# Performance work log

Measured on AMD Instinct MI355X. Metric: run time of the kernel, lower is better.

The kernel has to match this reference:

```python
import jax, jax.numpy as jnp
import numpy as np

EPS = 1e-7
LAMBDA_COORD = 10.0
LAMBDA_NOOBJ = 0.5
LAMBDA_OBJ = 1.0


def setup_inputs() -> dict:
    key = jax.random.key(0)
    k1, k2, k3, k4 = jax.random.split(key, 4)
    B, A, C, G = 64, 3, 20, 76
    predictions = jax.random.normal(k1, (B, A * (5 + C), G, G), dtype=jnp.float32) * 0.5
    txy = jax.random.uniform(k2, (B, A, G, G, 2), dtype=jnp.float32)
    twh = jax.random.normal(k3, (B, A, G, G, 2), dtype=jnp.float32) * 0.3
    tconf = (jax.random.uniform(k4, (B, A, G, G, 1), dtype=jnp.float32) < 0.05).astype(jnp.float32)
    targets = jnp.concatenate([txy, twh, tconf], axis=-1)
    anchors = jnp.array([[1.25, 1.625], [2.0, 3.75], [4.125, 2.875]], dtype=jnp.float32)
    return {"predictions": predictions, "targets": targets, "anchors": anchors}


def _bce(p, t):
    # elementwise binary cross-entropy; p in (0,1) from sigmoid
    return -(t * jnp.log(p) + (1.0 - t) * jnp.log1p(-p))


def _ciou_loss_elem(pb, tb):
    # pb, tb: [..., 4] corner boxes; returns elementwise (1 - ciou)
    x1p, y1p, x2p, y2p = pb[..., 0], pb[..., 1], pb[..., 2], pb[..., 3]
    x1t, y1t, x2t, y2t = tb[..., 0], tb[..., 1], tb[..., 2], tb[..., 3]
    iw = jnp.clip(jnp.minimum(x2p, x2t) - jnp.maximum(x1p, x1t), 0.0)
    ih = jnp.clip(jnp.minimum(y2p, y2t) - jnp.maximum(y1p, y1t), 0.0)
    inter = iw * ih
    area_p = jnp.clip(x2p - x1p, 0.0) * jnp.clip(y2p - y1p, 0.0)
    area_t = jnp.clip(x2t - x1t, 0.0) * jnp.clip(y2t - y1t, 0.0)
    union = area_p + area_t - inter + EPS
    iou = inter / union
    rho2 = ((x1p + x2p - x1t - x2t) * 0.5) ** 2 + ((y1p + y2p - y1t - y2t) * 0.5) ** 2
    en_w = jnp.clip(jnp.maximum(x2p, x2t) - jnp.minimum(x1p, x1t), EPS)
    en_h = jnp.clip(jnp.maximum(y2p, y2t) - jnp.minimum(y1p, y1t), EPS)
    c2 = en_w ** 2 + en_h ** 2
    w_p = jnp.clip(x2p - x1p, EPS); h_p = jnp.clip(y2p - y1p, EPS)
    w_t = jnp.clip(x2t - x1t, EPS); h_t = jnp.clip(y2t - y1t, EPS)
    v = (4.0 / (jnp.pi ** 2)) * (jnp.arctan(w_t / h_t) - jnp.arctan(w_p / h_p)) ** 2
    alpha = jax.lax.stop_gradient(v / (1.0 - iou + v + EPS))
    ciou = iou - rho2 / (c2 + EPS) - alpha * v
    return 1.0 - ciou


def reference(predictions, targets, anchors):
    B, Ch, G, _ = predictions.shape
    A = anchors.shape[0]
    C = Ch // A - 5
    p = predictions.reshape(B, A, 5 + C, G, G).transpose(0, 1, 3, 4, 2)  # [B,A,G,G,5+C]
    pred_xy = jax.nn.sigmoid(p[..., :2])
    pred_wh = p[..., 2:4]
    pred_conf = jax.nn.sigmoid(p[..., 4])
    pred_cls = jax.nn.sigmoid(p[..., 5:])
    obj = targets[..., 4] > 0          # [B,A,G,G]
    n_obj = jnp.sum(obj.astype(jnp.float32))
    n_noobj = jnp.sum((~obj).astype(jnp.float32))
    gy, gx = jnp.meshgrid(jnp.arange(G, dtype=jnp.float32), jnp.arange(G, dtype=jnp.float32), indexing='ij')
    inv_g = 1.0 / G
    aw = anchors[:, 0][None, :, None, None] * inv_g
    ah = anchors[:, 1][None, :, None, None] * inv_g
    # predicted corner boxes
    pcx = (gx + pred_xy[..., 0]) * inv_g
    pcy = (gy + pred_xy[..., 1]) * inv_g
    pw = jnp.exp(pred_wh[..., 0]) * aw
    ph = jnp.exp(pred_wh[..., 1]) * ah
    pred_corners = jnp.clip(jnp.stack([pcx - pw / 2, pcy - ph / 2, pcx + pw / 2, pcy + ph / 2], axis=-1), 0.0, 1.0)
    # target corner boxes
    tcx = (gx + targets[..., 0]) * inv_g
    tcy = (gy + targets[..., 1]) * inv_g
    tw = jnp.exp(targets[..., 2]) * aw
    th = jnp.exp(targets[..., 3]) * ah
    tgt_corners = jnp.clip(jnp.stack([tcx - tw / 2, tcy - th / 2, tcx + tw / 2, tcy + th / 2], axis=-1), 0.0, 1.0)
    ciou_l = _ciou_loss_elem(pred_corners, tgt_corners)  # [B,A,G,G]
    coord_sum = jnp.sum(jnp.where(obj, ciou_l, 0.0))
    coord_loss = jnp.where(n_obj > 0, coord_sum / jnp.maximum(n_obj, 1.0), 0.0)
    conf_bce = _bce(pred_conf, targets[..., 4])
    obj_loss = jnp.where(n_obj > 0, jnp.sum(jnp.where(obj, conf_bce, 0.0)) / jnp.maximum(n_obj, 1.0), 0.0)
    noobj_bce = -jnp.log1p(-pred_conf)  # BCE with target 0
    noobj_loss = jnp.where(n_noobj > 0, jnp.sum(jnp.where(~obj, noobj_bce, 0.0)) / jnp.maximum(n_noobj, 1.0), 0.0)
    if C > 0:
        cls_bce = -jnp.log(pred_cls)  # BCE with target 1
        cls_sum = jnp.sum(jnp.where(obj[..., None], cls_bce, 0.0))
        class_loss = jnp.where(n_obj > 0, cls_sum / jnp.maximum(n_obj * C, 1.0), 0.0)
    else:
        class_loss = jnp.float32(0.0)
    total = LAMBDA_COORD * coord_loss + LAMBDA_OBJ * obj_loss + LAMBDA_NOOBJ * noobj_loss + class_loss
    return total
```

## Files before the change

### kernel.cpp

```cpp
#include <hip/hip_runtime.h>
#include <math.h>

namespace {

constexpr int   kB     = 64;
constexpr int   kA     = 3;
constexpr int   kC     = 20;
constexpr int   kG     = 76;
constexpr int   kGG    = kG * kG;
constexpr int   kCH    = 5 + kC;
constexpr int   kNCell = kB * kA * kGG;
constexpr int   kNC4   = kNCell / 4;
constexpr int   kBlockA = 256;
constexpr int   kGridA  = kNC4 / kBlockA;
constexpr int   kCellsPerBlk = kBlockA * 4;
constexpr float kEps   = 1e-7f;
constexpr float kInvG  = 1.0f / (float)kG;

constexpr int kPart1Off = kGridA;
constexpr int kPart2Off = kGridA * 5;
constexpr int kListOff  = kGridA * 7;

__device__ __forceinline__ float softplus_fast(float x) {
  return fmaxf(x, 0.0f) + __logf(1.0f + __expf(-fabsf(x)));
}
__device__ __forceinline__ float sigmoidf(float x) {
  return 1.0f / (1.0f + __expf(-x));
}
__device__ __forceinline__ float clamp01(float x) {
  return fminf(fmaxf(x, 0.0f), 1.0f);
}

__device__ __forceinline__ void heavy_cell(
    int cell, const float* __restrict__ preds, const float* __restrict__ tgts,
    const float* __restrict__ anchors, float& coord, float& cls) {
  const int ba = cell / kGG;
  const int j  = cell - ba * kGG;
  const int a  = ba % kA;
  const int gy = j / kG;
  const int gx = j - gy * kG;
  const float fgx = (float)gx, fgy = (float)gy;

  const float aw = anchors[2 * a]     * kInvG;
  const float ah = anchors[2 * a + 1] * kInvG;

  const float* pb = preds + (size_t)ba * kCH * kGG + j;
  const float px  = pb[0];
  const float py  = pb[(size_t)1 * kGG];
  const float pwv = pb[(size_t)2 * kGG];
  const float phv = pb[(size_t)3 * kGG];

  const float* tc5 = tgts + (size_t)cell * 5;
  const float tx = tc5[0], ty = tc5[1], tw = tc5[2], th = tc5[3];

  const float pcx = (fgx + sigmoidf(px)) * kInvG;
  const float pcy = (fgy + sigmoidf(py)) * kInvG;
  const float pw  = __expf(pwv) * aw;
  const float ph  = __expf(phv) * ah;
  const float x1p = clamp01(pcx - 0.5f * pw);
  const float y1p = clamp01(pcy - 0.5f * ph);
  const float x2p = clamp01(pcx + 0.5f * pw);
  const float y2p = clamp01(pcy + 0.5f * ph);

  const float tcx = (fgx + tx) * kInvG;
  const float tcy = (fgy + ty) * kInvG;
  const float twv = __expf(tw) * aw;
  const float thv = __expf(th) * ah;
  const float x1t = clamp01(tcx - 0.5f * twv);
  const float y1t = clamp01(tcy - 0.5f * thv);
  const float x2t = clamp01(tcx + 0.5f * twv);
  const float y2t = clamp01(tcy + 0.5f * thv);

  const float iw     = fmaxf(fminf(x2p, x2t) - fmaxf(x1p, x1t), 0.0f);
  const float ih     = fmaxf(fminf(y2p, y2t) - fmaxf(y1p, y1t), 0.0f);
  const float inter  = iw * ih;
  const float area_p = fmaxf(x2p - x1p, 0.0f) * fmaxf(y2p - y1p, 0.0f);
  const float area_t = fmaxf(x2t - x1t, 0.0f) * fmaxf(y2t - y1t, 0.0f);
  const float uni    = area_p + area_t - inter + kEps;
  const float iou    = inter / uni;
  const float dx     = (x1p + x2p - x1t - x2t) * 0.5f;
  const float dy     = (y1p + y2p - y1t - y2t) * 0.5f;
  const float rho2   = dx * dx + dy * dy;
  const float enw    = fmaxf(fmaxf(x2p, x2t) - fminf(x1p, x1t), kEps);
  const float enh    = fmaxf(fmaxf(y2p, y2t) - fminf(y1p, y1t), kEps);
  const float c2     = enw * enw + enh * enh;
  const float wp     = fmaxf(x2p - x1p, kEps);
  const float hp     = fmaxf(y2p - y1p, kEps);
  const float wt     = fmaxf(x2t - x1t, kEps);
  const float ht     = fmaxf(y2t - y1t, kEps);
  const float k4pi2  = 4.0f / (float)(M_PI * M_PI);
  const float dat    = atanf(wt / ht) - atanf(wp / hp);
  const float v      = k4pi2 * dat * dat;
  const float alpha  = v / (1.0f - iou + v + kEps);
  const float ciou   = iou - rho2 / (c2 + kEps) - alpha * v;
  coord += 1.0f - ciou;

  float cacc = 0.0f;
  #pragma unroll
  for (int c = 0; c < kC; ++c) {
    cacc += softplus_fast(-pb[(size_t)(5 + c) * kGG]);
  }
  cls += cacc;
}

template <int N, int BLK>
__device__ __forceinline__ void block_reduceN(float r[N], float* out) {
  #pragma unroll
  for (int off = 32; off > 0; off >>= 1) {
    #pragma unroll
    for (int s = 0; s < N; ++s) r[s] += __shfl_down(r[s], off, 64);
  }
  __shared__ float red[BLK / 64][N];
  const int lane = threadIdx.x & 63;
  const int wid  = threadIdx.x >> 6;
  if (lane == 0) {
    #pragma unroll
    for (int s = 0; s < N; ++s) red[wid][s] = r[s];
  }
  __syncthreads();
  if (threadIdx.x == 0) {
    #pragma unroll
    for (int s = 0; s < N; ++s) {
      float acc = red[0][s];
      #pragma unroll
      for (int w = 1; w < BLK / 64; ++w) acc += red[w][s];
      out[s] = acc;
    }
  }
}

__global__ __launch_bounds__(kBlockA) void yolo_pass1(
    const float* __restrict__ preds,
    const float* __restrict__ tgts,
    const float* __restrict__ anchors,
    int* __restrict__ ws_i,
    int cap) {
  const int b    = blockIdx.x;
  const int q    = b * kBlockA + threadIdx.x;
  const int cell = q * 4;
  const int ba   = cell / kGG;
  const int j0   = cell - ba * kGG;

  const float4* tb = (const float4*)(tgts + (size_t)cell * 5);
  const float4 t1 = tb[1], t2 = tb[2], t3 = tb[3], t4 = tb[4];
  const float conf[4] = { t1.x, t2.y, t3.z, t4.w };

  const float* p4p = preds + (size_t)ba * kCH * kGG + (size_t)4 * kGG + j0;
  const float4 P4 = *(const float4*)p4p;
  const float p4a[4] = { P4.x, P4.y, P4.z, P4.w };

  float r[4] = {0.f, 0.f, 0.f, 0.f};
  unsigned msk = 0u;

  #pragma unroll
  for (int i = 0; i < 4; ++i) {
    const bool obj = conf[i] > 0.0f;
    const float sp = softplus_fast(p4a[i]);
    if (obj) {
      r[0] += sp - p4a[i];
      msk |= (1u << i);
    } else {
      r[1] += sp;
    }
  }
  const int cnt = __popc(msk);

  const int lane = threadIdx.x & 63;
  const int wid  = threadIdx.x >> 6;
  int incl = cnt;
  #pragma unroll
  for (int off = 1; off < 64; off <<= 1) {
    const int n = __shfl_up(incl, off, 64);
    if (lane >= off) incl += n;
  }
  const int excl = incl - cnt;

  __shared__ int wtot[kBlockA / 64];
  if (lane == 63) wtot[wid] = incl;
  __syncthreads();

  int wbase = 0;
  #pragma unroll
  for (int w = 0; w < kBlockA / 64; ++w) wbase += (w < wid) ? wtot[w] : 0;
  const int total = wtot[0] + wtot[1] + wtot[2] + wtot[3];

  if (threadIdx.x == 0) ws_i[b] = total;

  int* list = ws_i + kListOff + (size_t)b * cap;
  int p = wbase + excl;
  #pragma unroll
  for (int i = 0; i < 4; ++i) {
    if ((msk >> i) & 1u) {
      if (p < cap) {
        list[p] = cell + i;
      } else {
        heavy_cell(cell + i, preds, tgts, anchors, r[2], r[3]);
      }
      ++p;
    }
  }

  block_reduceN<4, kBlockA>(r, (float*)(ws_i + kPart1Off) + (size_t)b * 4);
}

__global__ __launch_bounds__(64) void yolo_pass2(
    const float* __restrict__ preds,
    const float* __restrict__ tgts,
    const float* __restrict__ anchors,
    int* __restrict__ ws_i,
    int cap) {
  const int b   = blockIdx.x;
  const int cnt = min(ws_i[b], cap);
  const int* list = ws_i + kListOff + (size_t)b * cap;

  float coord = 0.0f, cls = 0.0f;
  for (int i = threadIdx.x; i < cnt; i += 64) {
    heavy_cell(list[i], preds, tgts, anchors, coord, cls);
  }

  #pragma unroll
  for (int off = 32; off > 0; off >>= 1) {
    coord += __shfl_down(coord, off, 64);
    cls   += __shfl_down(cls,   off, 64);
  }
  if (threadIdx.x == 0) {
    float* p2 = (float*)(ws_i + kPart2Off) + (size_t)b * 2;
    p2[0] = coord;
    p2[1] = cls;
  }
}

__global__ __launch_bounds__(256) void yolo_finish(
    const int* __restrict__ ws_i, float* __restrict__ out) {
  const float* part1 = (const float*)(ws_i + kPart1Off);
  const float* part2 = (const float*)(ws_i + kPart2Off);

  float r[7] = {0.f, 0.f, 0.f, 0.f, 0.f, 0.f, 0.f};
  for (int i = threadIdx.x; i < kGridA; i += 256) {
    r[0] += (float)ws_i[i];
    r[1] += part1[(size_t)i * 4 + 0];
    r[2] += part1[(size_t)i * 4 + 1];
    r[3] += part1[(size_t)i * 4 + 2];
    r[4] += part1[(size_t)i * 4 + 3];
    r[5] += part2[(size_t)i * 2 + 0];
    r[6] += part2[(size_t)i * 2 + 1];
  }
  __shared__ float outbuf[7];
  block_reduceN<7, 256>(r, outbuf);
  __syncthreads();
  if (threadIdx.x == 0) {
    const float n_obj   = outbuf[0];
    const float objc    = outbuf[1];
    const float noobj   = outbuf[2];
    const float coord   = outbuf[3] + outbuf[5];
    const float cls     = outbuf[4] + outbuf[6];
    const float n_noobj = (float)kNCell - n_obj;

    const float coord_loss = (n_obj > 0.f)   ? coord / fmaxf(n_obj, 1.f)   : 0.f;
    const float obj_loss   = (n_obj > 0.f)   ? objc  / fmaxf(n_obj, 1.f)   : 0.f;
    const float noobj_loss = (n_noobj > 0.f) ? noobj / fmaxf(n_noobj, 1.f) : 0.f;
    const float class_loss = (n_obj > 0.f)   ? cls / fmaxf(n_obj * (float)kC, 1.f) : 0.f;

    out[0] = 10.0f * coord_loss + 1.0f * obj_loss + 0.5f * noobj_loss + class_loss;
  }
}

}

extern "C" void kernel_launch(void* const* d_in, const int* in_sizes, int n_in,
                              void* d_out, int out_size, void* d_ws, size_t ws_size,
                              hipStream_t stream) {
  const float* preds   = (const float*)d_in[0];
  const float* tgts    = (const float*)d_in[1];
  const float* anchors = (const float*)d_in[2];
  float* out = (float*)d_out;
  int*   ws  = (int*)d_ws;

  long words = (long)(ws_size / 4) - kListOff;
  int cap = (int)(words / kGridA);
  if (cap > kCellsPerBlk) cap = kCellsPerBlk;
  if (cap < 0) cap = 0;

  yolo_pass1<<<kGridA, kBlockA, 0, stream>>>(preds, tgts, anchors, ws, cap);
  yolo_pass2<<<kGridA, 64, 0, stream>>>(preds, tgts, anchors, ws, cap);
  yolo_finish<<<1, 256, 0, stream>>>(ws, out);
}
```

Before: 31.90 us.

## Fuse compaction and heavy CIoU pass into one kernel with LDS work list

Merges the two pass kernels into one. Each block compacts its object cells and their target xywh into shared memory, then processes that list with all 256 threads instead of a separate 64-thread kernel reading a global list. This drops a kernel launch, the global list round trip and the re-read of targets. It also replaces atanf and the precise divisions with a polynomial arctangent and fast divides, which changes numerical accuracy slightly.

```diff
diff --git a/kernel.cpp b/kernel.cpp
--- a/kernel.cpp
+++ b/kernel.cpp
@@ -16,10 +16,9 @@
 constexpr int   kCellsPerBlk = kBlockA * 4;
 constexpr float kEps   = 1e-7f;
 constexpr float kInvG  = 1.0f / (float)kG;
-
-constexpr int kPart1Off = kGridA;
-constexpr int kPart2Off = kGridA * 5;
-constexpr int kListOff  = kGridA * 7;
+constexpr float kPiO2  = 1.57079632679f;
+
+constexpr int kPartOff = kGridA;
 
 __device__ __forceinline__ float softplus_fast(float x) {
   return fmaxf(x, 0.0f) + __logf(1.0f + __expf(-fabsf(x)));
@@ -31,9 +30,22 @@
   return fminf(fmaxf(x, 0.0f), 1.0f);
 }
 
+__device__ __forceinline__ float atan_ratio(float num, float den) {
+  const float z  = __fdividef(fminf(num, den), fmaxf(num, den));
+  const float z2 = z * z;
+  float p = 0.0208351f;
+  p = fmaf(p, z2, -0.0851330f);
+  p = fmaf(p, z2,  0.1801410f);
+  p = fmaf(p, z2, -0.3302995f);
+  p = fmaf(p, z2,  0.9998660f);
+  const float a = z * p;
+  return (num > den) ? (kPiO2 - a) : a;
+}
+
 __device__ __forceinline__ void heavy_cell(
-    int cell, const float* __restrict__ preds, const float* __restrict__ tgts,
-    const float* __restrict__ anchors, float& coord, float& cls) {
+    int cell, float tx, float ty, float tw, float th,
+    const float* __restrict__ preds, const float* __restrict__ anchors,
+    float& coord, float& cls) {
   const int ba = cell / kGG;
   const int j  = cell - ba * kGG;
   const int a  = ba % kA;
@@ -49,9 +61,6 @@
   const float py  = pb[(size_t)1 * kGG];
   const float pwv = pb[(size_t)2 * kGG];
   const float phv = pb[(size_t)3 * kGG];
-
-  const float* tc5 = tgts + (size_t)cell * 5;
-  const float tx = tc5[0], ty = tc5[1], tw = tc5[2], th = tc5[3];
 
   const float pcx = (fgx + sigmoidf(px)) * kInvG;
   const float pcy = (fgy + sigmoidf(py)) * kInvG;
@@ -77,7 +86,7 @@
   const float area_p = fmaxf(x2p - x1p, 0.0f) * fmaxf(y2p - y1p, 0.0f);
   const float area_t = fmaxf(x2t - x1t, 0.0f) * fmaxf(y2t - y1t, 0.0f);
   const float uni    = area_p + area_t - inter + kEps;
-  const float iou    = inter / uni;
+  const float iou    = __fdividef(inter, uni);
   const float dx     = (x1p + x2p - x1t - x2t) * 0.5f;
   const float dy     = (y1p + y2p - y1t - y2t) * 0.5f;
   const float rho2   = dx * dx + dy * dy;
@@ -89,10 +98,10 @@
   const float wt     = fmaxf(x2t - x1t, kEps);
   const float ht     = fmaxf(y2t - y1t, kEps);
   const float k4pi2  = 4.0f / (float)(M_PI * M_PI);
-  const float dat    = atanf(wt / ht) - atanf(wp / hp);
+  const float dat    = atan_ratio(wt, ht) - atan_ratio(wp, hp);
   const float v      = k4pi2 * dat * dat;
-  const float alpha  = v / (1.0f - iou + v + kEps);
-  const float ciou   = iou - rho2 / (c2 + kEps) - alpha * v;
+  const float alpha  = __fdividef(v, 1.0f - iou + v + kEps);
+  const float ciou   = iou - __fdividef(rho2, c2 + kEps) - alpha * v;
   coord += 1.0f - ciou;
 
   float cacc = 0.0f;
@@ -129,21 +138,25 @@
   }
 }
 
-__global__ __launch_bounds__(kBlockA) void yolo_pass1(
+__global__ __launch_bounds__(kBlockA) void yolo_fused(
     const float* __restrict__ preds,
     const float* __restrict__ tgts,
     const float* __restrict__ anchors,
-    int* __restrict__ ws_i,
-    int cap) {
+    int* __restrict__ ws_i) {
+  __shared__ int    s_list[kCellsPerBlk];
+  __shared__ float4 s_tgt[kCellsPerBlk];
+  __shared__ int    s_wtot[kBlockA / 64];
+
   const int b    = blockIdx.x;
   const int q    = b * kBlockA + threadIdx.x;
   const int cell = q * 4;
   const int ba   = cell / kGG;
   const int j0   = cell - ba * kGG;
 
+  union { float4 v[5]; float f[20]; } T;
   const float4* tb = (const float4*)(tgts + (size_t)cell * 5);
-  const float4 t1 = tb[1], t2 = tb[2], t3 = tb[3], t4 = tb[4];
-  const float conf[4] = { t1.x, t2.y, t3.z, t4.w };
+  #pragma unroll
+  for (int i = 0; i < 5; ++i) T.v[i] = tb[i];
 
   const float* p4p = preds + (size_t)ba * kCH * kGG + (size_t)4 * kGG + j0;
   const float4 P4 = *(const float4*)p4p;
@@ -154,7 +167,7 @@
 
   #pragma unroll
   for (int i = 0; i < 4; ++i) {
-    const bool obj = conf[i] > 0.0f;
+    const bool obj = T.f[i * 5 + 4] > 0.0f;
     const float sp = softplus_fast(p4a[i]);
     if (obj) {
       r[0] += sp - p4a[i];
@@ -175,85 +188,58 @@
   }
   const int excl = incl - cnt;
 
-  __shared__ int wtot[kBlockA / 64];
-  if (lane == 63) wtot[wid] = incl;
+  if (lane == 63) s_wtot[wid] = incl;
   __syncthreads();
 
   int wbase = 0;
   #pragma unroll
-  for (int w = 0; w < kBlockA / 64; ++w) wbase += (w < wid) ? wtot[w] : 0;
-  const int total = wtot[0] + wtot[1] + wtot[2] + wtot[3];
+  for (int w = 0; w < kBlockA / 64; ++w) wbase += (w < wid) ? s_wtot[w] : 0;
+  const int total = s_wtot[0] + s_wtot[1] + s_wtot[2] + s_wtot[3];
 
   if (threadIdx.x == 0) ws_i[b] = total;
 
-  int* list = ws_i + kListOff + (size_t)b * cap;
   int p = wbase + excl;
   #pragma unroll
   for (int i = 0; i < 4; ++i) {
     if ((msk >> i) & 1u) {
-      if (p < cap) {
-        list[p] = cell + i;
-      } else {
-        heavy_cell(cell + i, preds, tgts, anchors, r[2], r[3]);
-      }
+      s_list[p] = cell + i;
+      s_tgt[p]  = make_float4(T.f[i * 5 + 0], T.f[i * 5 + 1],
+                              T.f[i * 5 + 2], T.f[i * 5 + 3]);
       ++p;
     }
   }
-
-  block_reduceN<4, kBlockA>(r, (float*)(ws_i + kPart1Off) + (size_t)b * 4);
-}
-
-__global__ __launch_bounds__(64) void yolo_pass2(
-    const float* __restrict__ preds,
-    const float* __restrict__ tgts,
-    const float* __restrict__ anchors,
-    int* __restrict__ ws_i,
-    int cap) {
-  const int b   = blockIdx.x;
-  const int cnt = min(ws_i[b], cap);
-  const int* list = ws_i + kListOff + (size_t)b * cap;
-
-  float coord = 0.0f, cls = 0.0f;
-  for (int i = threadIdx.x; i < cnt; i += 64) {
-    heavy_cell(list[i], preds, tgts, anchors, coord, cls);
-  }
-
-  #pragma unroll
-  for (int off = 32; off > 0; off >>= 1) {
-    coord += __shfl_down(coord, off, 64);
-    cls   += __shfl_down(cls,   off, 64);
-  }
-  if (threadIdx.x == 0) {
-    float* p2 = (float*)(ws_i + kPart2Off) + (size_t)b * 2;
-    p2[0] = coord;
-    p2[1] = cls;
-  }
+  __syncthreads();
+
+  for (int i = threadIdx.x; i < total; i += kBlockA) {
+    const int c  = s_list[i];
+    const float4 t4 = s_tgt[i];
+    heavy_cell(c, t4.x, t4.y, t4.z, t4.w, preds, anchors, r[2], r[3]);
+  }
+
+  block_reduceN<4, kBlockA>(r, (float*)(ws_i + kPartOff) + (size_t)b * 4);
 }
 
 __global__ __launch_bounds__(256) void yolo_finish(
     const int* __restrict__ ws_i, float* __restrict__ out) {
-  const float* part1 = (const float*)(ws_i + kPart1Off);
-  const float* part2 = (const float*)(ws_i + kPart2Off);
-
-  float r[7] = {0.f, 0.f, 0.f, 0.f, 0.f, 0.f, 0.f};
+  const float* part = (const float*)(ws_i + kPartOff);
+
+  float r[5] = {0.f, 0.f, 0.f, 0.f, 0.f};
   for (int i = threadIdx.x; i < kGridA; i += 256) {
     r[0] += (float)ws_i[i];
-    r[1] += part1[(size_t)i * 4 + 0];
-    r[2] += part1[(size_t)i * 4 + 1];
-    r[3] += part1[(size_t)i * 4 + 2];
-    r[4] += part1[(size_t)i * 4 + 3];
-    r[5] += part2[(size_t)i * 2 + 0];
-    r[6] += part2[(size_t)i * 2 + 1];
-  }
-  __shared__ float outbuf[7];
-  block_reduceN<7, 256>(r, outbuf);
+    r[1] += part[(size_t)i * 4 + 0];
+    r[2] += part[(size_t)i * 4 + 1];
+    r[3] += part[(size_t)i * 4 + 2];
+    r[4] += part[(size_t)i * 4 + 3];
+  }
+  __shared__ float outbuf[5];
+  block_reduceN<5, 256>(r, outbuf);
   __syncthreads();
   if (threadIdx.x == 0) {
     const float n_obj   = outbuf[0];
     const float objc    = outbuf[1];
     const float noobj   = outbuf[2];
-    const float coord   = outbuf[3] + outbuf[5];
-    const float cls     = outbuf[4] + outbuf[6];
+    const float coord   = outbuf[3];
+    const float cls     = outbuf[4];
     const float n_noobj = (float)kNCell - n_obj;
 
     const float coord_loss = (n_obj > 0.f)   ? coord / fmaxf(n_obj, 1.f)   : 0.f;
@@ -276,12 +262,6 @@
   float* out = (float*)d_out;
   int*   ws  = (int*)d_ws;
 
-  long words = (long)(ws_size / 4) - kListOff;
-  int cap = (int)(words / kGridA);
-  if (cap > kCellsPerBlk) cap = kCellsPerBlk;
-  if (cap < 0) cap = 0;
-
-  yolo_pass1<<<kGridA, kBlockA, 0, stream>>>(preds, tgts, anchors, ws, cap);
-  yolo_pass2<<<kGridA, 64, 0, stream>>>(preds, tgts, anchors, ws, cap);
+  yolo_fused<<<kGridA, kBlockA, 0, stream>>>(preds, tgts, anchors, ws);
   yolo_finish<<<1, 256, 0, stream>>>(ws, out);
 }
```

After: 27.05 us. -15.2%, faster.
